# Kernel optimization log

Measured on AMD Instinct MI355X. Metric: run time of the kernel, lower is better.

The kernel has to match this reference:

```python
import jax, jax.numpy as jnp
import numpy as np

B, T, D, V, L = 32, 512, 512, 1024, 128
BLANK = 0
NEG = -1e30  # log-domain 'minus infinity' that is fp-safe


def setup_inputs() -> dict:
    key = jax.random.key(0)
    k1, k2, k3 = jax.random.split(key, 3)
    x = jax.random.normal(k1, (B, T, D), dtype=jnp.float32)
    W = jax.random.normal(k2, (D, V), dtype=jnp.float32) / np.sqrt(D).astype(np.float32)
    b = jnp.zeros((V,), dtype=jnp.float32)
    # CTC targets must be in [1, V) (never the blank id 0)
    target = jax.random.randint(k3, (B, L), 1, V)
    input_lengths = jnp.full((B,), T, dtype=jnp.int32)
    target_lengths = jnp.full((B,), L, dtype=jnp.int32)
    return {"x": x, "W": W, "b": b, "target": target,
            "input_lengths": input_lengths, "target_lengths": target_lengths}


def _ctc_loss(log_probs, target, input_lengths, target_lengths):
    # log_probs: [T, B, V] (time-major), target: [B, L]
    Tt, Bb, _ = log_probs.shape
    Ll = target.shape[1]
    S = 2 * Ll + 1  # extended label sequence: blank,t0,blank,t1,...,blank
    ext = jnp.full((Bb, S), BLANK, dtype=target.dtype).at[:, 1::2].set(target)  # [B,S]
    ext_m2 = jnp.pad(ext, ((0, 0), (2, 0)), constant_values=BLANK)[:, :S]
    skip = (ext != BLANK) & (ext != ext_m2) & (jnp.arange(S)[None, :] >= 2)  # [B,S]

    # gather log-probs of extended labels for every time step: [T,B,S]
    lp_ext = jnp.take_along_axis(log_probs, jnp.broadcast_to(ext[None], (Tt, Bb, S)), axis=2)

    alpha0 = jnp.full((Bb, S), NEG, log_probs.dtype)
    alpha0 = alpha0.at[:, 0].set(lp_ext[0, :, 0]).at[:, 1].set(lp_ext[0, :, 1])

    def step(alpha, lp_t):
        a1 = jnp.pad(alpha, ((0, 0), (1, 0)), constant_values=NEG)[:, :S]
        a2 = jnp.pad(alpha, ((0, 0), (2, 0)), constant_values=NEG)[:, :S]
        c = jnp.logaddexp(alpha, a1)
        c = jnp.where(skip, jnp.logaddexp(c, a2), c)
        new = c + lp_t
        return new, new

    _, alphas = jax.lax.scan(step, alpha0, lp_ext[1:])
    alphas = jnp.concatenate([alpha0[None], alphas], axis=0)  # [T,B,S]

    bi = jnp.arange(Bb)
    a_last = alphas[input_lengths - 1, bi]  # [B,S] alpha at each sample's final frame
    ll = jnp.logaddexp(a_last[bi, 2 * target_lengths - 1], a_last[bi, 2 * target_lengths])
    nll = -ll  # per-sample negative log-likelihood
    # zero_infinity=True: infinite losses are zeroed
    nll = jnp.where(jnp.isinf(nll) | (nll > 1e29), 0.0, nll)
    # reduction='mean': divide each loss by its target length, then mean
    return jnp.mean(nll / jnp.maximum(target_lengths, 1).astype(nll.dtype))


def reference(x, W, b, target, input_lengths, target_lengths):
    logits = jnp.einsum('btd,dv->btv', x, W) + b  # nn.Linear
    log_probs = jax.nn.log_softmax(logits, axis=-1)  # [B,T,V]
    return _ctc_loss(jnp.transpose(log_probs, (1, 0, 2)), target, input_lengths, target_lengths)
```

## Files before the change

kernel.cpp:

```cpp
#include <hip/hip_runtime.h>
#include <cstdint>


#define SPAD 260
#define PEXT_PAD_ROWS 64
#define ASTR 520
#define L2E 1.4426950408889634f
#define LN2 0.6931471805599453f

typedef short v8s __attribute__((ext_vector_type(8)));
typedef float v4f __attribute__((ext_vector_type(4)));

__device__ __forceinline__ uint32_t f2bf_bits(float f) {
  uint32_t u = __float_as_uint(f);
  return (u + 0x7FFFu + ((u >> 16) & 1u)) >> 16;
}
__device__ __forceinline__ float bf2f(uint32_t h) { return __uint_as_float(h << 16); }

__global__ void k_prep(const float* __restrict__ x, uint16_t* __restrict__ xb, long long n,
                       const float* __restrict__ W, uint16_t* __restrict__ Wt, int D, int V,
                       float* __restrict__ out, int nconv) {
  if (blockIdx.x == 0 && threadIdx.x == 0) out[0] = 0.f;
  if ((int)blockIdx.x < nconv) {
    long long i = ((long long)blockIdx.x * blockDim.x + threadIdx.x) * 8;
    if (i >= n) return;
    float4 a = *(const float4*)(x + i);
    float4 b = *(const float4*)(x + i + 4);
    uint4 o;
    o.x = f2bf_bits(a.x) | (f2bf_bits(a.y) << 16);
    o.y = f2bf_bits(a.z) | (f2bf_bits(a.w) << 16);
    o.z = f2bf_bits(b.x) | (f2bf_bits(b.y) << 16);
    o.w = f2bf_bits(b.z) | (f2bf_bits(b.w) << 16);
    *(uint4*)(xb + i) = o;
  } else {
    __shared__ float tile[32][33];
    const int bid2 = blockIdx.x - nconv;
    const int n0 = (bid2 % (V / 32)) * 32, k0 = (bid2 / (V / 32)) * 32;
    const int tx = threadIdx.x & 31, ty = threadIdx.x >> 5;
    #pragma unroll
    for (int i = 0; i < 32; i += 8)
      tile[ty + i][tx] = W[(size_t)(k0 + ty + i) * V + n0 + tx];
    __syncthreads();
    #pragma unroll
    for (int i = 0; i < 32; i += 8)
      Wt[(size_t)(n0 + ty + i) * D + k0 + tx] = (uint16_t)f2bf_bits(tile[tx][ty + i]);
  }
}

__global__ __launch_bounds__(256) void k_gemm(const uint16_t* __restrict__ A,
                                              const uint16_t* __restrict__ Bt,
                                              const float* __restrict__ bias,
                                              uint16_t* __restrict__ C, int M, int N, int K) {
  __shared__ uint16_t As[64 * ASTR];
  const int tid = threadIdx.x, lane = tid & 63, wave = tid >> 6;
  const int m0 = blockIdx.x * 64, n0 = blockIdx.y * 256;
  const int frow = lane & 15, kb = lane >> 4;
  v4f acc[4][4] = {};

  #pragma unroll
  for (int i = 0; i < 16; i++) {
    const int r = i * 4 + wave;
    const uint16_t* ga = A + (size_t)(m0 + r) * K + lane * 8;
    __builtin_amdgcn_global_load_lds(
        (const __attribute__((address_space(1))) void*)ga,
        (__attribute__((address_space(3))) void*)(As + r * ASTR + lane * 8), 16, 0, 0);
  }
  __syncthreads();

  const uint16_t* Bw = Bt + (size_t)(n0 + wave * 64) * K;
  #pragma unroll 2
  for (int k0 = 0; k0 < K; k0 += 32) {
    v8s bfr[4], af[4];
    #pragma unroll
    for (int j = 0; j < 4; j++)
      bfr[j] = *(const v8s*)(Bw + (size_t)(j * 16 + frow) * K + k0 + kb * 8);
    #pragma unroll
    for (int i = 0; i < 4; i++)
      af[i] = *(const v8s*)(As + (i * 16 + frow) * ASTR + k0 + kb * 8);
    #pragma unroll
    for (int i = 0; i < 4; i++)
      #pragma unroll
      for (int j = 0; j < 4; j++)
        acc[i][j] = __builtin_amdgcn_mfma_f32_16x16x32_bf16(af[i], bfr[j], acc[i][j], 0, 0, 0);
  }

  const int crow = (lane >> 4) * 4, ccol = lane & 15;
  #pragma unroll
  for (int j = 0; j < 4; j++) {
    const int n = n0 + wave * 64 + j * 16 + ccol;
    const float bv = bias[n];
    #pragma unroll
    for (int i = 0; i < 4; i++) {
      const int mb = m0 + i * 16 + crow;
      #pragma unroll
      for (int r2 = 0; r2 < 4; r2++)
        C[(size_t)(mb + r2) * N + n] = (uint16_t)f2bf_bits(acc[i][j][r2] + bv);
    }
  }
}

__global__ void k_softmax_gather(const uint16_t* __restrict__ logits, const int* __restrict__ target,
                                 const int* __restrict__ tlen, float* __restrict__ pext,
                                 int T, int V, int L) {
  const int row = blockIdx.x * 4 + (threadIdx.x >> 6);
  const int lane = threadIdx.x & 63;
  const uint16_t* lrow = logits + (size_t)row * V;

  float xs[16];
  int cnt = 0;
  float mx = -INFINITY;
  for (int base = 0; base < V; base += 256) {
    const int idx = base + lane * 4;
    uint2 u = *(const uint2*)(lrow + idx);
    float4 v;
    v.x = bf2f(u.x & 0xFFFFu); v.y = bf2f(u.x >> 16);
    v.z = bf2f(u.y & 0xFFFFu); v.w = bf2f(u.y >> 16);
    xs[cnt] = v.x; xs[cnt + 1] = v.y; xs[cnt + 2] = v.z; xs[cnt + 3] = v.w; cnt += 4;
    mx = fmaxf(mx, fmaxf(fmaxf(v.x, v.y), fmaxf(v.z, v.w)));
  }
  #pragma unroll
  for (int off = 32; off; off >>= 1) mx = fmaxf(mx, __shfl_xor(mx, off, 64));
  float sum = 0.f;
  #pragma unroll
  for (int q = 0; q < 16; q++) { if (q < cnt) sum += exp2f((xs[q] - mx) * L2E); }
  #pragma unroll
  for (int off = 32; off; off >>= 1) sum += __shfl_xor(sum, off, 64);
  const float lse2 = mx * L2E + log2f(sum);

  const int bidx = row / T;
  const int Lb = tlen[bidx];
  const int S = 2 * Lb + 1;
  float* prow = pext + (size_t)row * SPAD;
  for (int s = lane; s < SPAD; s += 64) {
    float p = 0.f;
    if (s < S) {
      const int lbl = (s & 1) ? target[bidx * L + ((s - 1) >> 1)] : 0;
      p = exp2f(bf2f(lrow[lbl]) * L2E - lse2);
    }
    prow[s] = p;
  }
}

__device__ __forceinline__ float wave_shr1(float x) {
  return __int_as_float(__builtin_amdgcn_update_dpp(0, __float_as_int(x), 0x138, 0xf, 0xf, true));
}
__device__ __forceinline__ float wave_max_nonneg(float x) {
  x = fmaxf(x, __int_as_float(__builtin_amdgcn_update_dpp(0, __float_as_int(x), 0x111, 0xf, 0xf, true)));
  x = fmaxf(x, __int_as_float(__builtin_amdgcn_update_dpp(0, __float_as_int(x), 0x112, 0xf, 0xf, true)));
  x = fmaxf(x, __int_as_float(__builtin_amdgcn_update_dpp(0, __float_as_int(x), 0x114, 0xf, 0xf, true)));
  x = fmaxf(x, __int_as_float(__builtin_amdgcn_update_dpp(0, __float_as_int(x), 0x118, 0xf, 0xf, true)));
  x = fmaxf(x, __int_as_float(__builtin_amdgcn_update_dpp(0, __float_as_int(x), 0x142, 0xf, 0xf, true)));
  x = fmaxf(x, __int_as_float(__builtin_amdgcn_update_dpp(0, __float_as_int(x), 0x143, 0xf, 0xf, true)));
  return __int_as_float(__builtin_amdgcn_readlane(__float_as_int(x), 63));
}

__device__ __forceinline__ void load8(float4* __restrict__ p, float* __restrict__ p4,
                                      const float* __restrict__ pb, int t0, int lane) {
  #pragma unroll
  for (int k = 0; k < 8; k++) {
    const float* row = pb + (size_t)(t0 + k) * SPAD;
    p[k] = *(const float4*)(row + (lane << 2));
    p4[k] = row[256];
  }
}

__global__ __launch_bounds__(64, 1) void k_ctc(const float* __restrict__ pext,
                                               const int* __restrict__ target,
                                               const int* __restrict__ ilen,
                                               const int* __restrict__ tlen,
                                               float* __restrict__ out, int T, int L) {
  const int b = blockIdx.x;
  const int lane = threadIdx.x;
  const int B = gridDim.x;
  const int Tb = ilen[b];
  const int Lb = tlen[b];
  const int S = 2 * Lb + 1;
  const int* tg = target + b * L;

  const int s1 = 4 * lane + 1, s3 = 4 * lane + 3;
  float sk1 = 0.f, sk3 = 0.f;
  if (s1 >= 3 && s1 < S) sk1 = (tg[(s1 - 1) >> 1] != tg[(s1 - 3) >> 1]) ? 1.f : 0.f;
  if (s3 >= 3 && s3 < S) sk3 = (tg[(s3 - 1) >> 1] != tg[(s3 - 3) >> 1]) ? 1.f : 0.f;

  const float* pb = pext + (size_t)b * T * SPAD;
  const float4 p0 = *(const float4*)(pb + (lane << 2));
  float a0 = (lane == 0) ? p0.x : 0.f;
  float a1 = (lane == 0) ? p0.y : 0.f;
  float a2 = 0.f, a3 = 0.f, a4 = 0.f;
  float log2C = 0.f;

  #define CTC_STEP(PP, P4) {                                            \
    const float pm3 = wave_shr1(a3);                                    \
    const float a255 = __int_as_float(__builtin_amdgcn_readlane(__float_as_int(a3), 63)); \
    const float n0v = (a0 + pm3) * (PP).x;                              \
    const float n1v = (a1 + a0 + sk1 * pm3) * (PP).y;                   \
    const float n2v = (a2 + a1) * (PP).z;                               \
    const float n3v = (a3 + a2 + sk3 * a1) * (PP).w;                    \
    const float n4v = (a4 + a255) * (P4);                               \
    a0 = n0v; a1 = n1v; a2 = n2v; a3 = n3v; a4 = n4v; }

  #define RENORM {                                                      \
    float m = fmaxf(fmaxf(fmaxf(a0, a1), fmaxf(a2, a3)), a4);           \
    m = wave_max_nonneg(m);                                             \
    const int e = (int)((__float_as_uint(m) >> 23) & 255u) - 127;       \
    const float scale = __uint_as_float((uint32_t)(127 - e) << 23);     \
    a0 *= scale; a1 *= scale; a2 *= scale; a3 *= scale; a4 *= scale;    \
    log2C += (float)e; }

  float4 Pa[8], Pb_[8], Pc[8], Pd[8];
  float Qa[8], Qb[8], Qc[8], Qd[8];
  int t0 = 1;
  bool done = false;
  load8(Pa, Qa, pb, t0, lane);
  load8(Pb_, Qb, pb, t0 + 8, lane);
  load8(Pc, Qc, pb, t0 + 16, lane);
  __builtin_amdgcn_sched_barrier(0);

  #define PHASE(LP, LQ, CP, CQ) {                                       \
    if (t0 + 8 <= Tb) {                                                 \
      load8(LP, LQ, pb, t0 + 24, lane);                                 \
      __builtin_amdgcn_sched_barrier(0);                                \
      _Pragma("unroll")                                                 \
      for (int k = 0; k < 8; k++) CTC_STEP(CP[k], CQ[k]);               \
      RENORM; t0 += 8;                                                  \
    } else {                                                            \
      _Pragma("unroll")                                                 \
      for (int k = 0; k < 8; k++) { if (t0 + k < Tb) CTC_STEP(CP[k], CQ[k]); } \
      RENORM; done = true;                                              \
    } }

  while (!done) {
    PHASE(Pd, Qd, Pa, Qa); if (done) break;
    PHASE(Pa, Qa, Pb_, Qb); if (done) break;
    PHASE(Pb_, Qb, Pc, Qc); if (done) break;
    PHASE(Pc, Qc, Pd, Qd);
  }

  __shared__ float abuf[257];
  abuf[4 * lane + 0] = a0; abuf[4 * lane + 1] = a1;
  abuf[4 * lane + 2] = a2; abuf[4 * lane + 3] = a3;
  if (lane == 63) abuf[256] = a4;
  __syncthreads();
  if (lane == 0) {
    const float ssum = abuf[2 * Lb - 1] + abuf[2 * Lb];
    const float ll = (log2f(ssum) + log2C) * LN2;
    float nll = -ll;
    if (!(nll < 1e29f)) nll = 0.f;
    atomicAdd(out, nll / ((float)(Lb > 0 ? Lb : 1) * (float)B));
  }
}

extern "C" void kernel_launch(void* const* d_in, const int* in_sizes, int n_in,
                              void* d_out, int out_size, void* d_ws, size_t ws_size,
                              hipStream_t stream) {
  const float* x      = (const float*)d_in[0];
  const float* W      = (const float*)d_in[1];
  const float* bias   = (const float*)d_in[2];
  const int*  target  = (const int*)d_in[3];
  const int*  ilen    = (const int*)d_in[4];
  const int*  tlen    = (const int*)d_in[5];

  const int B = in_sizes[4];
  const int V = in_sizes[2];
  const int D = in_sizes[1] / V;
  const int T = in_sizes[0] / (B * D);
  const int L = in_sizes[3] / B;
  const int M = B * T;

  char* ws = (char*)d_ws;
  const size_t xb_bytes = (size_t)M * D * 2;
  const size_t wt_bytes = (size_t)V * D * 2;
  const size_t pext_bytes = (size_t)(M + PEXT_PAD_ROWS) * SPAD * 4;
  uint16_t* xb = (uint16_t*)ws;
  uint16_t* Wt = (uint16_t*)(ws + xb_bytes);
  uint16_t* logits = (uint16_t*)(ws + xb_bytes + wt_bytes);
  const size_t log_bytes = (size_t)M * V * 2;

  float* pext;
  if (pext_bytes <= xb_bytes + wt_bytes) {
    pext = (float*)ws;
  } else {
    pext = (float*)(ws + xb_bytes + wt_bytes + log_bytes);
  }

  const long long nx = (long long)M * D;
  const int nconv = (int)((nx / 8 + 255) / 256);
  const int ntrans = (V / 32) * (D / 32);
  k_prep<<<nconv + ntrans, 256, 0, stream>>>(x, xb, nx, W, Wt, D, V, (float*)d_out, nconv);
  k_gemm<<<dim3(M / 64, V / 256), 256, 0, stream>>>(xb, Wt, bias, logits, M, V, D);
  k_softmax_gather<<<M / 4, 256, 0, stream>>>(logits, target, tlen, pext, T, V, L);
  k_ctc<<<B, 64, 0, stream>>>(pext, target, ilen, tlen, (float*)d_out, T, L);
}
```

Before: 182.6 us.

## Fuse GEMM, log-softmax and label gather into one full-vocab block kernel

Replaces the separate GEMM (which wrote bf16 logits to global memory) and softmax/gather kernels with one kernel. Each 1024-thread block computes a 64-row by full-vocabulary tile, reduces max and sum across waves through shared memory, and writes the gathered extended-label probabilities straight from the accumulators. This removes the logits round trip and a kernel launch. In exchange it runs a block-wide label loop in which every wave scans all targets, and occupancy is limited to one large block per CU.

```diff
diff --git a/kernel.cpp b/kernel.cpp
--- a/kernel.cpp
+++ b/kernel.cpp
@@ -4,7 +4,6 @@
 
 #define SPAD 260
 #define PEXT_PAD_ROWS 64
-#define ASTR 520
 #define L2E 1.4426950408889634f
 #define LN2 0.6931471805599453f
 
@@ -47,36 +46,47 @@
   }
 }
 
-__global__ __launch_bounds__(256) void k_gemm(const uint16_t* __restrict__ A,
-                                              const uint16_t* __restrict__ Bt,
-                                              const float* __restrict__ bias,
-                                              uint16_t* __restrict__ C, int M, int N, int K) {
-  __shared__ uint16_t As[64 * ASTR];
+__global__ __launch_bounds__(1024, 1) void k_fused(const uint16_t* __restrict__ A,
+                                                   const uint16_t* __restrict__ Bt,
+                                                   const float* __restrict__ bias,
+                                                   const int* __restrict__ target,
+                                                   const int* __restrict__ tlen,
+                                                   float* __restrict__ pext,
+                                                   int T, int K, int L) {
+  extern __shared__ char smem[];
+  const int astr = K + 8;
+  uint16_t* As = (uint16_t*)smem;
+  float* red_mx = (float*)(smem + (size_t)64 * astr * 2);
+  float* red_sm = red_mx + 64 * 16;
+  float* lse2s  = red_sm + 64 * 16;
+  float* pblank = lse2s + 64;
+
   const int tid = threadIdx.x, lane = tid & 63, wave = tid >> 6;
-  const int m0 = blockIdx.x * 64, n0 = blockIdx.y * 256;
-  const int frow = lane & 15, kb = lane >> 4;
+  const int ccol = lane & 15, q = lane >> 4;
+  const int m0 = blockIdx.x * 64;
+
+  #pragma unroll
+  for (int i = 0; i < 4; i++) {
+    const int r = wave * 4 + i;
+    for (int kc = 0; kc < K; kc += 512) {
+      const uint16_t* ga = A + (size_t)(m0 + r) * K + kc + lane * 8;
+      __builtin_amdgcn_global_load_lds(
+          (const __attribute__((address_space(1))) void*)ga,
+          (__attribute__((address_space(3))) void*)(As + r * astr + kc + lane * 8), 16, 0, 0);
+    }
+  }
+  __syncthreads();
+
+  const uint16_t* Bw = Bt + (size_t)(wave * 64) * K;
   v4f acc[4][4] = {};
-
-  #pragma unroll
-  for (int i = 0; i < 16; i++) {
-    const int r = i * 4 + wave;
-    const uint16_t* ga = A + (size_t)(m0 + r) * K + lane * 8;
-    __builtin_amdgcn_global_load_lds(
-        (const __attribute__((address_space(1))) void*)ga,
-        (__attribute__((address_space(3))) void*)(As + r * ASTR + lane * 8), 16, 0, 0);
-  }
-  __syncthreads();
-
-  const uint16_t* Bw = Bt + (size_t)(n0 + wave * 64) * K;
-  #pragma unroll 2
   for (int k0 = 0; k0 < K; k0 += 32) {
     v8s bfr[4], af[4];
     #pragma unroll
     for (int j = 0; j < 4; j++)
-      bfr[j] = *(const v8s*)(Bw + (size_t)(j * 16 + frow) * K + k0 + kb * 8);
+      bfr[j] = *(const v8s*)(Bw + (size_t)(j * 16 + ccol) * K + k0 + q * 8);
     #pragma unroll
     for (int i = 0; i < 4; i++)
-      af[i] = *(const v8s*)(As + (i * 16 + frow) * ASTR + k0 + kb * 8);
+      af[i] = *(const v8s*)(As + (i * 16 + ccol) * astr + k0 + q * 8);
     #pragma unroll
     for (int i = 0; i < 4; i++)
       #pragma unroll
@@ -84,60 +94,87 @@
         acc[i][j] = __builtin_amdgcn_mfma_f32_16x16x32_bf16(af[i], bfr[j], acc[i][j], 0, 0, 0);
   }
 
-  const int crow = (lane >> 4) * 4, ccol = lane & 15;
-  #pragma unroll
-  for (int j = 0; j < 4; j++) {
-    const int n = n0 + wave * 64 + j * 16 + ccol;
-    const float bv = bias[n];
-    #pragma unroll
-    for (int i = 0; i < 4; i++) {
-      const int mb = m0 + i * 16 + crow;
-      #pragma unroll
-      for (int r2 = 0; r2 < 4; r2++)
-        C[(size_t)(mb + r2) * N + n] = (uint16_t)f2bf_bits(acc[i][j][r2] + bv);
+  float bv[4];
+  #pragma unroll
+  for (int j = 0; j < 4; j++) bv[j] = bias[wave * 64 + j * 16 + ccol];
+  #pragma unroll
+  for (int i = 0; i < 4; i++)
+    #pragma unroll
+    for (int j = 0; j < 4; j++)
+      #pragma unroll
+      for (int r2 = 0; r2 < 4; r2++) acc[i][j][r2] += bv[j];
+
+  #pragma unroll
+  for (int i = 0; i < 4; i++)
+    #pragma unroll
+    for (int r2 = 0; r2 < 4; r2++) {
+      float m = fmaxf(fmaxf(acc[i][0][r2], acc[i][1][r2]), fmaxf(acc[i][2][r2], acc[i][3][r2]));
+      #pragma unroll
+      for (int off = 1; off < 16; off <<= 1) m = fmaxf(m, __shfl_xor(m, off, 64));
+      float s = 0.f;
+      #pragma unroll
+      for (int j = 0; j < 4; j++) s += exp2f((acc[i][j][r2] - m) * L2E);
+      #pragma unroll
+      for (int off = 1; off < 16; off <<= 1) s += __shfl_xor(s, off, 64);
+      if (ccol == 0) {
+        const int row = i * 16 + 4 * q + r2;
+        red_mx[row * 16 + wave] = m;
+        red_sm[row * 16 + wave] = s;
+      }
     }
-  }
-}
-
-__global__ void k_softmax_gather(const uint16_t* __restrict__ logits, const int* __restrict__ target,
-                                 const int* __restrict__ tlen, float* __restrict__ pext,
-                                 int T, int V, int L) {
-  const int row = blockIdx.x * 4 + (threadIdx.x >> 6);
-  const int lane = threadIdx.x & 63;
-  const uint16_t* lrow = logits + (size_t)row * V;
-
-  float xs[16];
-  int cnt = 0;
-  float mx = -INFINITY;
-  for (int base = 0; base < V; base += 256) {
-    const int idx = base + lane * 4;
-    uint2 u = *(const uint2*)(lrow + idx);
-    float4 v;
-    v.x = bf2f(u.x & 0xFFFFu); v.y = bf2f(u.x >> 16);
-    v.z = bf2f(u.y & 0xFFFFu); v.w = bf2f(u.y >> 16);
-    xs[cnt] = v.x; xs[cnt + 1] = v.y; xs[cnt + 2] = v.z; xs[cnt + 3] = v.w; cnt += 4;
-    mx = fmaxf(mx, fmaxf(fmaxf(v.x, v.y), fmaxf(v.z, v.w)));
-  }
-  #pragma unroll
-  for (int off = 32; off; off >>= 1) mx = fmaxf(mx, __shfl_xor(mx, off, 64));
-  float sum = 0.f;
-  #pragma unroll
-  for (int q = 0; q < 16; q++) { if (q < cnt) sum += exp2f((xs[q] - mx) * L2E); }
-  #pragma unroll
-  for (int off = 32; off; off >>= 1) sum += __shfl_xor(sum, off, 64);
-  const float lse2 = mx * L2E + log2f(sum);
-
-  const int bidx = row / T;
-  const int Lb = tlen[bidx];
+  __syncthreads();
+
+  if (tid < 64) {
+    float M = -INFINITY;
+    #pragma unroll
+    for (int w = 0; w < 16; w++) M = fmaxf(M, red_mx[tid * 16 + w]);
+    float S = 0.f;
+    #pragma unroll
+    for (int w = 0; w < 16; w++) S += red_sm[tid * 16 + w] * exp2f((red_mx[tid * 16 + w] - M) * L2E);
+    lse2s[tid] = M * L2E + log2f(S);
+  }
+  __syncthreads();
+
+  if (wave == 0 && ccol == 0) {
+    #pragma unroll
+    for (int i = 0; i < 4; i++)
+      #pragma unroll
+      for (int r2 = 0; r2 < 4; r2++) {
+        const int row = i * 16 + 4 * q + r2;
+        pblank[row] = exp2f(acc[i][0][r2] * L2E - lse2s[row]);
+      }
+  }
+
+  const int b = m0 / T;
+  const int Lb = tlen[b];
   const int S = 2 * Lb + 1;
-  float* prow = pext + (size_t)row * SPAD;
-  for (int s = lane; s < SPAD; s += 64) {
-    float p = 0.f;
-    if (s < S) {
-      const int lbl = (s & 1) ? target[bidx * L + ((s - 1) >> 1)] : 0;
-      p = exp2f(bf2f(lrow[lbl]) * L2E - lse2);
+  const int* tg = target + b * L;
+  for (int li = 0; li < Lb; li++) {
+    const int lbl = tg[li];
+    if ((lbl >> 6) != wave) continue;
+    if (ccol == (lbl & 15)) {
+      const int j = (lbl >> 4) & 3;
+      #pragma unroll
+      for (int i = 0; i < 4; i++)
+        #pragma unroll
+        for (int r2 = 0; r2 < 4; r2++) {
+          const int row = i * 16 + 4 * q + r2;
+          pext[(size_t)(m0 + row) * SPAD + 2 * li + 1] =
+              exp2f(acc[i][j][r2] * L2E - lse2s[row]);
+        }
     }
-    prow[s] = p;
+  }
+  __syncthreads();
+
+  #pragma unroll
+  for (int rr = 0; rr < 4; rr++) {
+    const int row = wave * 4 + rr;
+    const float pb = pblank[row];
+    float* prow = pext + (size_t)(m0 + row) * SPAD;
+    for (int s = lane; s < SPAD; s += 64) {
+      if (s >= S)       prow[s] = 0.f;
+      else if (!(s & 1)) prow[s] = pb;
+    }
   }
 }
 
@@ -270,24 +307,18 @@
   char* ws = (char*)d_ws;
   const size_t xb_bytes = (size_t)M * D * 2;
   const size_t wt_bytes = (size_t)V * D * 2;
-  const size_t pext_bytes = (size_t)(M + PEXT_PAD_ROWS) * SPAD * 4;
   uint16_t* xb = (uint16_t*)ws;
   uint16_t* Wt = (uint16_t*)(ws + xb_bytes);
-  uint16_t* logits = (uint16_t*)(ws + xb_bytes + wt_bytes);
-  const size_t log_bytes = (size_t)M * V * 2;
-
-  float* pext;
-  if (pext_bytes <= xb_bytes + wt_bytes) {
-    pext = (float*)ws;
-  } else {
-    pext = (float*)(ws + xb_bytes + wt_bytes + log_bytes);
-  }
+  float* pext = (float*)(ws + xb_bytes + wt_bytes);
 
   const long long nx = (long long)M * D;
   const int nconv = (int)((nx / 8 + 255) / 256);
   const int ntrans = (V / 32) * (D / 32);
   k_prep<<<nconv + ntrans, 256, 0, stream>>>(x, xb, nx, W, Wt, D, V, (float*)d_out, nconv);
-  k_gemm<<<dim3(M / 64, V / 256), 256, 0, stream>>>(xb, Wt, bias, logits, M, V, D);
-  k_softmax_gather<<<M / 4, 256, 0, stream>>>(logits, target, tlen, pext, T, V, L);
+
+  const int smem = 64 * (D + 8) * 2 + 64 * 16 * 4 * 2 + 64 * 4 * 2;
+  hipFuncSetAttribute((const void*)k_fused, hipFuncAttributeMaxDynamicSharedMemorySize, smem);
+  k_fused<<<M / 64, 1024, smem, stream>>>(xb, Wt, bias, target, tlen, pext, T, D, L);
+
   k_ctc<<<B, 64, 0, stream>>>(pext, target, ilen, tlen, (float*)d_out, T, L);
 }
```

Result: slower. 212.7 us (+16.5%).
